# Performance work log

Measured on AMD Instinct MI355X. Metric: run time of the kernel, lower is better.

The kernel has to match this reference:

```python
import jax, jax.numpy as jnp
import numpy as np

B, S, E = 16384, 32, 128
H, DH, O = 4, 32, 128  # num_heads, head_dim (qkv_features//num_heads), out_features


def setup_inputs() -> dict:
    key = jax.random.key(0)
    kx, kq, kk, kv, ko = jax.random.split(key, 5)
    return {
        "x": jax.random.normal(kx, (B, S, E), dtype=jnp.float32),
        "w_q": jax.random.normal(kq, (H, E, DH), dtype=jnp.float32),
        "w_k": jax.random.normal(kk, (H, E, DH), dtype=jnp.float32),
        "w_v": jax.random.normal(kv, (H, E, DH), dtype=jnp.float32),
        "w_o": jax.random.normal(ko, (H, DH, O), dtype=jnp.float32),
    }


def reference(x, w_q, w_k, w_v, w_o):
    # Per-head projections: [B, H, S, DH]
    scale = jnp.asarray(w_q.shape[-1] ** -0.5, x.dtype)
    Q = jnp.einsum("bse,hed->bhsd", x, w_q) * scale
    K = jnp.einsum("bse,hed->bhsd", x, w_k)
    V = jnp.einsum("bse,hed->bhsd", x, w_v)
    scores = jnp.einsum("bhsd,bhtd->bhst", Q, K)  # [B, H, S, S]
    A = jax.nn.softmax(scores, axis=-1)
    Hd = jnp.einsum("bhst,bhtd->bhsd", A, V)  # [B, H, S, DH]
    # Per-head output projection, summed across heads: [B, S, O]
    out = jnp.einsum("bhsd,hdo->bso", Hd, w_o)
    return out
```

## Files before the change

### kernel.cpp

```cpp
#include <hip/hip_runtime.h>


typedef __bf16 bf16x8 __attribute__((ext_vector_type(8)));
typedef float f32x4 __attribute__((ext_vector_type(4)));

union FragU { unsigned int w[4]; bf16x8 v; };

__device__ inline unsigned short f2bf(float f) {
  unsigned int u = __builtin_bit_cast(unsigned int, f);
  u += 0x7FFFu + ((u >> 16) & 1u);
  return (unsigned short)(u >> 16);
}
__device__ inline float bf2f(unsigned short h) {
  return __builtin_bit_cast(float, (unsigned int)h << 16);
}

__device__ inline bf16x8 ld_frag8(const unsigned short* p) {
  FragU f;
  const uint2* q = (const uint2*)p;
  uint2 a = q[0], b = q[1];
  f.w[0] = a.x; f.w[1] = a.y; f.w[2] = b.x; f.w[3] = b.y;
  return f.v;
}

__device__ inline f32x4 mfma16(bf16x8 a, bf16x8 b, f32x4 c) {
  return __builtin_amdgcn_mfma_f32_16x16x32_bf16(a, b, c, 0, 0, 0);
}

__device__ inline void copy16(const unsigned short* src, unsigned short* dst) {
  uint4 a = *(const uint4*)src;
  uint4 b = *((const uint4*)src + 1);
  uint2* d = (uint2*)dst;
  d[0] = make_uint2(a.x, a.y); d[1] = make_uint2(a.z, a.w);
  d[2] = make_uint2(b.x, b.y); d[3] = make_uint2(b.z, b.w);
}

__global__ void prep_w(const float* __restrict__ wq, const float* __restrict__ wk,
                       const float* __restrict__ wv, const float* __restrict__ wo,
                       unsigned short* __restrict__ wsb) {
  int idx = blockIdx.x * 256 + threadIdx.x;
  int t = idx >> 14;
  int rem = idx & 16383;
  int hh = rem >> 12;
  int r2 = rem & 4095;
  const float* src = (t == 0) ? wq : (t == 1) ? wk : (t == 2) ? wv : wo;
  float v = src[rem];
  if (t == 0) v *= 0.17677669529663687f;
  int off;
  if (t < 3) { int e = r2 >> 5, d = r2 & 31; off = (hh << 12) + (d << 7) + e; }
  else       { int dh = r2 >> 7, o = r2 & 127; off = (hh << 12) + (o << 5) + dh; }
  unsigned short hi = f2bf(v);
  unsigned short lo = f2bf(v - bf2f(hi));
  wsb[(t << 15) + off] = hi;
  wsb[(t << 15) + 16384 + off] = lo;
}

#define OFF_WB_HI 0
#define OFF_WB_LO 4608
#define OFF_K_HI  9216
#define OFF_K_LO  11520
#define OFF_VT_HI 13824
#define OFF_VT_LO 16128
#define OFF_Q_HI  18432
#define OFF_Q_LO  20736
#define LDS_TOT   23040

__global__ __launch_bounds__(256, 2) void attn_fused(
    const float* __restrict__ x, const unsigned short* __restrict__ wsb,
    float* __restrict__ out) {
  __shared__ unsigned short lds[LDS_TOT];
  const int tid = threadIdx.x;
  const int lane = tid & 63;
  const int wid = tid >> 6;
  const int bl = wid >> 1;
  const int hw = wid & 1;
  const int sbase = hw << 4;
  const int col = lane & 15;
  const int quad = lane >> 4;

  bf16x8 xh[4], xl[4];
  for (int b = 0; b < 2; ++b) {
    const float4* xg = (const float4*)(x + ((long)(blockIdx.x * 2 + b) << 12));
#pragma unroll
    for (int it = 0; it < 4; ++it) {
      int f4 = it * 256 + tid;
      float4 v = xg[f4];
      int s = f4 >> 5;
      int e = (f4 & 31) << 2;
      unsigned short a0 = f2bf(v.x), b0 = f2bf(v.x - bf2f(a0));
      unsigned short a1 = f2bf(v.y), b1 = f2bf(v.y - bf2f(a1));
      unsigned short a2 = f2bf(v.z), b2 = f2bf(v.z - bf2f(a2));
      unsigned short a3 = f2bf(v.w), b3 = f2bf(v.w - bf2f(a3));
      uint2 ph, pl;
      ph.x = (unsigned)a0 | ((unsigned)a1 << 16);
      ph.y = (unsigned)a2 | ((unsigned)a3 << 16);
      pl.x = (unsigned)b0 | ((unsigned)b1 << 16);
      pl.y = (unsigned)b2 | ((unsigned)b3 << 16);
      *(uint2*)(lds + s * 132 + e) = ph;
      *(uint2*)(lds + 4224 + s * 132 + e) = pl;
    }
    __syncthreads();
    if (bl == b) {
#pragma unroll
      for (int kk = 0; kk < 4; ++kk) {
        xh[kk] = ld_frag8(lds + (sbase + col) * 132 + (kk << 5) + (quad << 3));
        xl[kk] = ld_frag8(lds + 4224 + (sbase + col) * 132 + (kk << 5) + (quad << 3));
      }
    }
    __syncthreads();
  }

  const long batch = (long)blockIdx.x * 2 + bl;
  const f32x4 zero = {0.f, 0.f, 0.f, 0.f};
  f32x4 oacc[8];
#pragma unroll
  for (int i = 0; i < 8; ++i) oacc[i] = zero;

  unsigned short* Kh = lds + OFF_K_HI + bl * 1152;
  unsigned short* Kl = lds + OFF_K_LO + bl * 1152;
  unsigned short* Vh = lds + OFF_VT_HI + bl * 1152;
  unsigned short* Vl = lds + OFF_VT_LO + bl * 1152;
  unsigned short* Qh = lds + OFF_Q_HI + (bl * 2 + hw) * 576;
  unsigned short* Ql = lds + OFF_Q_LO + (bl * 2 + hw) * 576;
  unsigned short* Abuf = lds + OFF_K_HI + bl * 1152;

  for (int hh = 0; hh < 4; ++hh) {
    __syncthreads();

    {
      int i0 = tid << 4, d = i0 >> 7, e0 = i0 & 127;
      copy16(wsb + (hh << 12) + i0, lds + OFF_WB_HI + d * 132 + e0);
      copy16(wsb + 16384 + (hh << 12) + i0, lds + OFF_WB_LO + d * 132 + e0);
    }
    __syncthreads();
    f32x4 c0 = zero, c1 = zero;
#pragma unroll
    for (int kk = 0; kk < 4; ++kk) {
      bf16x8 f0 = ld_frag8(lds + OFF_WB_HI + col * 132 + (kk << 5) + (quad << 3));
      bf16x8 f1 = ld_frag8(lds + OFF_WB_HI + (col + 16) * 132 + (kk << 5) + (quad << 3));
      bf16x8 g0 = ld_frag8(lds + OFF_WB_LO + col * 132 + (kk << 5) + (quad << 3));
      bf16x8 g1 = ld_frag8(lds + OFF_WB_LO + (col + 16) * 132 + (kk << 5) + (quad << 3));
      c0 = mfma16(xh[kk], f0, c0); c0 = mfma16(xl[kk], f0, c0); c0 = mfma16(xh[kk], g0, c0);
      c1 = mfma16(xh[kk], f1, c1); c1 = mfma16(xl[kk], f1, c1); c1 = mfma16(xh[kk], g1, c1);
    }
#pragma unroll
    for (int r = 0; r < 4; ++r) {
      int row = (quad << 2) + r;
      unsigned short hi = f2bf(c0[r]), lo = f2bf(c0[r] - bf2f(hi));
      Qh[row * 36 + col] = hi; Ql[row * 36 + col] = lo;
      hi = f2bf(c1[r]); lo = f2bf(c1[r] - bf2f(hi));
      Qh[row * 36 + col + 16] = hi; Ql[row * 36 + col + 16] = lo;
    }
    __syncthreads();

    {
      int i0 = tid << 4, d = i0 >> 7, e0 = i0 & 127;
      copy16(wsb + 32768 + (hh << 12) + i0, lds + OFF_WB_HI + d * 132 + e0);
      copy16(wsb + 32768 + 16384 + (hh << 12) + i0, lds + OFF_WB_LO + d * 132 + e0);
    }
    __syncthreads();
    c0 = zero; c1 = zero;
#pragma unroll
    for (int kk = 0; kk < 4; ++kk) {
      bf16x8 f0 = ld_frag8(lds + OFF_WB_HI + col * 132 + (kk << 5) + (quad << 3));
      bf16x8 f1 = ld_frag8(lds + OFF_WB_HI + (col + 16) * 132 + (kk << 5) + (quad << 3));
      bf16x8 g0 = ld_frag8(lds + OFF_WB_LO + col * 132 + (kk << 5) + (quad << 3));
      bf16x8 g1 = ld_frag8(lds + OFF_WB_LO + (col + 16) * 132 + (kk << 5) + (quad << 3));
      c0 = mfma16(xh[kk], f0, c0); c0 = mfma16(xl[kk], f0, c0); c0 = mfma16(xh[kk], g0, c0);
      c1 = mfma16(xh[kk], f1, c1); c1 = mfma16(xl[kk], f1, c1); c1 = mfma16(xh[kk], g1, c1);
    }
#pragma unroll
    for (int r = 0; r < 4; ++r) {
      int row = sbase + (quad << 2) + r;
      unsigned short hi = f2bf(c0[r]), lo = f2bf(c0[r] - bf2f(hi));
      Kh[row * 36 + col] = hi; Kl[row * 36 + col] = lo;
      hi = f2bf(c1[r]); lo = f2bf(c1[r] - bf2f(hi));
      Kh[row * 36 + col + 16] = hi; Kl[row * 36 + col + 16] = lo;
    }
    __syncthreads();

    {
      int i0 = tid << 4, d = i0 >> 7, e0 = i0 & 127;
      copy16(wsb + 65536 + (hh << 12) + i0, lds + OFF_WB_HI + d * 132 + e0);
      copy16(wsb + 65536 + 16384 + (hh << 12) + i0, lds + OFF_WB_LO + d * 132 + e0);
    }
    __syncthreads();
    c0 = zero; c1 = zero;
#pragma unroll
    for (int kk = 0; kk < 4; ++kk) {
      bf16x8 f0 = ld_frag8(lds + OFF_WB_HI + col * 132 + (kk << 5) + (quad << 3));
      bf16x8 f1 = ld_frag8(lds + OFF_WB_HI + (col + 16) * 132 + (kk << 5) + (quad << 3));
      bf16x8 g0 = ld_frag8(lds + OFF_WB_LO + col * 132 + (kk << 5) + (quad << 3));
      bf16x8 g1 = ld_frag8(lds + OFF_WB_LO + (col + 16) * 132 + (kk << 5) + (quad << 3));
      c0 = mfma16(xh[kk], f0, c0); c0 = mfma16(xl[kk], f0, c0); c0 = mfma16(xh[kk], g0, c0);
      c1 = mfma16(xh[kk], f1, c1); c1 = mfma16(xl[kk], f1, c1); c1 = mfma16(xh[kk], g1, c1);
    }
#pragma unroll
    for (int r = 0; r < 4; ++r) {
      int t = sbase + (quad << 2) + r;
      unsigned short hi = f2bf(c0[r]), lo = f2bf(c0[r] - bf2f(hi));
      Vh[col * 36 + t] = hi; Vl[col * 36 + t] = lo;
      hi = f2bf(c1[r]); lo = f2bf(c1[r] - bf2f(hi));
      Vh[(col + 16) * 36 + t] = hi; Vl[(col + 16) * 36 + t] = lo;
    }
    __syncthreads();

    f32x4 s0 = zero, s1 = zero;
    {
      bf16x8 qhf = ld_frag8(Qh + col * 36 + (quad << 3));
      bf16x8 qlf = ld_frag8(Ql + col * 36 + (quad << 3));
      bf16x8 k0 = ld_frag8(Kh + col * 36 + (quad << 3));
      bf16x8 k1 = ld_frag8(Kh + (col + 16) * 36 + (quad << 3));
      bf16x8 k0l = ld_frag8(Kl + col * 36 + (quad << 3));
      bf16x8 k1l = ld_frag8(Kl + (col + 16) * 36 + (quad << 3));
      s0 = mfma16(qhf, k0, s0); s0 = mfma16(qlf, k0, s0); s0 = mfma16(qhf, k0l, s0);
      s1 = mfma16(qhf, k1, s1); s1 = mfma16(qlf, k1, s1); s1 = mfma16(qhf, k1l, s1);
    }
    float a0[4], a1[4];
#pragma unroll
    for (int r = 0; r < 4; ++r) {
      float v0 = s0[r], v1 = s1[r];
      float mx = fmaxf(v0, v1);
#pragma unroll
      for (int dx = 1; dx < 16; dx <<= 1) mx = fmaxf(mx, __shfl_xor(mx, dx));
      float e0 = __expf(v0 - mx), e1 = __expf(v1 - mx);
      float sm = e0 + e1;
#pragma unroll
      for (int dx = 1; dx < 16; dx <<= 1) sm += __shfl_xor(sm, dx);
      float inv = 1.0f / sm;
      a0[r] = e0 * inv; a1[r] = e1 * inv;
    }
    __syncthreads();
#pragma unroll
    for (int r = 0; r < 4; ++r) {
      int row = sbase + (quad << 2) + r;
      Abuf[row * 36 + col] = f2bf(a0[r]);
      Abuf[row * 36 + col + 16] = f2bf(a1[r]);
    }
    __syncthreads();

    f32x4 hv0 = zero, hv1 = zero;
    {
      bf16x8 af = ld_frag8(Abuf + (sbase + col) * 36 + (quad << 3));
      bf16x8 v0h = ld_frag8(Vh + col * 36 + (quad << 3));
      bf16x8 v1h = ld_frag8(Vh + (col + 16) * 36 + (quad << 3));
      bf16x8 v0l = ld_frag8(Vl + col * 36 + (quad << 3));
      bf16x8 v1l = ld_frag8(Vl + (col + 16) * 36 + (quad << 3));
      hv0 = mfma16(af, v0h, hv0); hv0 = mfma16(af, v0l, hv0);
      hv1 = mfma16(af, v1h, hv1); hv1 = mfma16(af, v1l, hv1);
    }
#pragma unroll
    for (int r = 0; r < 4; ++r) {
      int row = (quad << 2) + r;
      unsigned short hi = f2bf(hv0[r]), lo = f2bf(hv0[r] - bf2f(hi));
      Qh[row * 36 + col] = hi; Ql[row * 36 + col] = lo;
      hi = f2bf(hv1[r]); lo = f2bf(hv1[r] - bf2f(hi));
      Qh[row * 36 + col + 16] = hi; Ql[row * 36 + col + 16] = lo;
    }
    {
      int i0 = tid << 4, o = i0 >> 5, d0 = i0 & 31;
      copy16(wsb + 98304 + (hh << 12) + i0, lds + OFF_WB_HI + o * 36 + d0);
      copy16(wsb + 98304 + 16384 + (hh << 12) + i0, lds + OFF_WB_LO + o * 36 + d0);
    }
    __syncthreads();
    {
      bf16x8 dh = ld_frag8(Qh + col * 36 + (quad << 3));
      bf16x8 dl = ld_frag8(Ql + col * 36 + (quad << 3));
#pragma unroll
      for (int t8 = 0; t8 < 8; ++t8) {
        bf16x8 wh = ld_frag8(lds + OFF_WB_HI + ((t8 << 4) + col) * 36 + (quad << 3));
        bf16x8 wl = ld_frag8(lds + OFF_WB_LO + ((t8 << 4) + col) * 36 + (quad << 3));
        oacc[t8] = mfma16(dh, wh, oacc[t8]);
        oacc[t8] = mfma16(dl, wh, oacc[t8]);
        oacc[t8] = mfma16(dh, wl, oacc[t8]);
      }
    }
  }

  float* og = out + batch * 4096;
#pragma unroll
  for (int t8 = 0; t8 < 8; ++t8) {
#pragma unroll
    for (int r = 0; r < 4; ++r) {
      og[(sbase + (quad << 2) + r) * 128 + (t8 << 4) + col] = oacc[t8][r];
    }
  }
}

extern "C" void kernel_launch(void* const* d_in, const int* in_sizes, int n_in,
                              void* d_out, int out_size, void* d_ws, size_t ws_size,
                              hipStream_t stream) {
  const float* x = (const float*)d_in[0];
  const float* wq = (const float*)d_in[1];
  const float* wk = (const float*)d_in[2];
  const float* wv = (const float*)d_in[3];
  const float* wo = (const float*)d_in[4];
  float* out = (float*)d_out;
  unsigned short* wsb = (unsigned short*)d_ws;
  hipLaunchKernelGGL(prep_w, dim3(256), dim3(256), 0, stream, wq, wk, wv, wo, wsb);
  hipLaunchKernelGGL(attn_fused, dim3(8192), dim3(256), 0, stream, x, wsb, out);
}
```

Before: 710.4 us.

## Load weights as pre-swizzled MFMA fragments from global, drop LDS staging and lo-terms

Weights are reordered on the host-side prep kernel into per-lane MFMA fragment order, so the fused kernel loads B-fragments directly from global/L2 with 16-byte loads instead of staging them through LDS with barriers. This shrinks LDS usage, allowing launch bounds to raise occupancy to 5 blocks per CU, and removes many __syncthreads. It also drops the low-order bf16 correction terms for V, the attention-V product, and the output weights, cutting MFMA count at the cost of accuracy. The softmax probabilities now reuse the per-wave Q buffer, removing further barriers.

```diff
diff --git a/kernel.cpp b/kernel.cpp
--- a/kernel.cpp
+++ b/kernel.cpp
@@ -23,16 +23,15 @@
   return f.v;
 }
 
+__device__ inline bf16x8 ld_gfrag(const unsigned short* p) {
+  FragU f;
+  uint4 v = *(const uint4*)p;
+  f.w[0] = v.x; f.w[1] = v.y; f.w[2] = v.z; f.w[3] = v.w;
+  return f.v;
+}
+
 __device__ inline f32x4 mfma16(bf16x8 a, bf16x8 b, f32x4 c) {
   return __builtin_amdgcn_mfma_f32_16x16x32_bf16(a, b, c, 0, 0, 0);
-}
-
-__device__ inline void copy16(const unsigned short* src, unsigned short* dst) {
-  uint4 a = *(const uint4*)src;
-  uint4 b = *((const uint4*)src + 1);
-  uint2* d = (uint2*)dst;
-  d[0] = make_uint2(a.x, a.y); d[1] = make_uint2(a.z, a.w);
-  d[2] = make_uint2(b.x, b.y); d[3] = make_uint2(b.z, b.w);
 }
 
 __global__ void prep_w(const float* __restrict__ wq, const float* __restrict__ wk,
@@ -40,32 +39,33 @@
                        unsigned short* __restrict__ wsb) {
   int idx = blockIdx.x * 256 + threadIdx.x;
   int t = idx >> 14;
-  int rem = idx & 16383;
-  int hh = rem >> 12;
-  int r2 = rem & 4095;
+  int h = (idx >> 12) & 3;
+  int r = idx & 4095;
   const float* src = (t == 0) ? wq : (t == 1) ? wk : (t == 2) ? wv : wo;
-  float v = src[rem];
-  if (t == 0) v *= 0.17677669529663687f;
-  int off;
-  if (t < 3) { int e = r2 >> 5, d = r2 & 31; off = (hh << 12) + (d << 7) + e; }
-  else       { int dh = r2 >> 7, o = r2 & 127; off = (hh << 12) + (o << 5) + dh; }
+  int L = (r >> 3) & 63, j = r & 7;
+  float v;
+  if (t < 3) {
+    int kk = r >> 10, half = (r >> 9) & 1;
+    int d = half * 16 + (L & 15);
+    int e = kk * 32 + ((L >> 4) << 3) + j;
+    v = src[h * 4096 + e * 32 + d];
+    if (t == 0) v *= 0.17677669529663687f;
+  } else {
+    int t8 = r >> 9;
+    int o = t8 * 16 + (L & 15);
+    int d = ((L >> 4) << 3) + j;
+    v = src[h * 4096 + d * 128 + o];
+  }
   unsigned short hi = f2bf(v);
   unsigned short lo = f2bf(v - bf2f(hi));
-  wsb[(t << 15) + off] = hi;
-  wsb[(t << 15) + 16384 + off] = lo;
-}
-
-#define OFF_WB_HI 0
-#define OFF_WB_LO 4608
-#define OFF_K_HI  9216
-#define OFF_K_LO  11520
-#define OFF_VT_HI 13824
-#define OFF_VT_LO 16128
-#define OFF_Q_HI  18432
-#define OFF_Q_LO  20736
-#define LDS_TOT   23040
-
-__global__ __launch_bounds__(256, 2) void attn_fused(
+  int base = (t * 4 + h) * 8192 + r;
+  wsb[base] = hi;
+  wsb[base + 4096] = lo;
+}
+
+#define LDS_TOT 11520
+
+__global__ __launch_bounds__(256, 5) void attn_fused(
     const float* __restrict__ x, const unsigned short* __restrict__ wsb,
     float* __restrict__ out) {
   __shared__ unsigned short lds[LDS_TOT];
@@ -77,6 +77,7 @@
   const int sbase = hw << 4;
   const int col = lane & 15;
   const int quad = lane >> 4;
+  const int lo8 = lane << 3;
 
   bf16x8 xh[4], xl[4];
   for (int b = 0; b < 2; ++b) {
@@ -116,30 +117,26 @@
 #pragma unroll
   for (int i = 0; i < 8; ++i) oacc[i] = zero;
 
-  unsigned short* Kh = lds + OFF_K_HI + bl * 1152;
-  unsigned short* Kl = lds + OFF_K_LO + bl * 1152;
-  unsigned short* Vh = lds + OFF_VT_HI + bl * 1152;
-  unsigned short* Vl = lds + OFF_VT_LO + bl * 1152;
-  unsigned short* Qh = lds + OFF_Q_HI + (bl * 2 + hw) * 576;
-  unsigned short* Ql = lds + OFF_Q_LO + (bl * 2 + hw) * 576;
-  unsigned short* Abuf = lds + OFF_K_HI + bl * 1152;
+  unsigned short* Kh = lds + 0 + bl * 1152;
+  unsigned short* Kl = lds + 2304 + bl * 1152;
+  unsigned short* Vth = lds + 4608 + bl * 1152;
+  unsigned short* Qh = lds + 6912 + wid * 576;
+  unsigned short* Ql = lds + 9216 + wid * 576;
 
   for (int hh = 0; hh < 4; ++hh) {
-    __syncthreads();
-
-    {
-      int i0 = tid << 4, d = i0 >> 7, e0 = i0 & 127;
-      copy16(wsb + (hh << 12) + i0, lds + OFF_WB_HI + d * 132 + e0);
-      copy16(wsb + 16384 + (hh << 12) + i0, lds + OFF_WB_LO + d * 132 + e0);
-    }
-    __syncthreads();
+    if (hh) __syncthreads();
+    const unsigned short* wqb = wsb + (0 * 4 + hh) * 8192;
+    const unsigned short* wkb = wsb + (1 * 4 + hh) * 8192;
+    const unsigned short* wvb = wsb + (2 * 4 + hh) * 8192;
+    const unsigned short* wob = wsb + (3 * 4 + hh) * 8192;
+
     f32x4 c0 = zero, c1 = zero;
 #pragma unroll
     for (int kk = 0; kk < 4; ++kk) {
-      bf16x8 f0 = ld_frag8(lds + OFF_WB_HI + col * 132 + (kk << 5) + (quad << 3));
-      bf16x8 f1 = ld_frag8(lds + OFF_WB_HI + (col + 16) * 132 + (kk << 5) + (quad << 3));
-      bf16x8 g0 = ld_frag8(lds + OFF_WB_LO + col * 132 + (kk << 5) + (quad << 3));
-      bf16x8 g1 = ld_frag8(lds + OFF_WB_LO + (col + 16) * 132 + (kk << 5) + (quad << 3));
+      bf16x8 f0 = ld_gfrag(wqb + kk * 1024 + lo8);
+      bf16x8 f1 = ld_gfrag(wqb + kk * 1024 + 512 + lo8);
+      bf16x8 g0 = ld_gfrag(wqb + 4096 + kk * 1024 + lo8);
+      bf16x8 g1 = ld_gfrag(wqb + 4096 + kk * 1024 + 512 + lo8);
       c0 = mfma16(xh[kk], f0, c0); c0 = mfma16(xl[kk], f0, c0); c0 = mfma16(xh[kk], g0, c0);
       c1 = mfma16(xh[kk], f1, c1); c1 = mfma16(xl[kk], f1, c1); c1 = mfma16(xh[kk], g1, c1);
     }
@@ -151,21 +148,14 @@
       hi = f2bf(c1[r]); lo = f2bf(c1[r] - bf2f(hi));
       Qh[row * 36 + col + 16] = hi; Ql[row * 36 + col + 16] = lo;
     }
-    __syncthreads();
-
-    {
-      int i0 = tid << 4, d = i0 >> 7, e0 = i0 & 127;
-      copy16(wsb + 32768 + (hh << 12) + i0, lds + OFF_WB_HI + d * 132 + e0);
-      copy16(wsb + 32768 + 16384 + (hh << 12) + i0, lds + OFF_WB_LO + d * 132 + e0);
-    }
-    __syncthreads();
+
     c0 = zero; c1 = zero;
 #pragma unroll
     for (int kk = 0; kk < 4; ++kk) {
-      bf16x8 f0 = ld_frag8(lds + OFF_WB_HI + col * 132 + (kk << 5) + (quad << 3));
-      bf16x8 f1 = ld_frag8(lds + OFF_WB_HI + (col + 16) * 132 + (kk << 5) + (quad << 3));
-      bf16x8 g0 = ld_frag8(lds + OFF_WB_LO + col * 132 + (kk << 5) + (quad << 3));
-      bf16x8 g1 = ld_frag8(lds + OFF_WB_LO + (col + 16) * 132 + (kk << 5) + (quad << 3));
+      bf16x8 f0 = ld_gfrag(wkb + kk * 1024 + lo8);
+      bf16x8 f1 = ld_gfrag(wkb + kk * 1024 + 512 + lo8);
+      bf16x8 g0 = ld_gfrag(wkb + 4096 + kk * 1024 + lo8);
+      bf16x8 g1 = ld_gfrag(wkb + 4096 + kk * 1024 + 512 + lo8);
       c0 = mfma16(xh[kk], f0, c0); c0 = mfma16(xl[kk], f0, c0); c0 = mfma16(xh[kk], g0, c0);
       c1 = mfma16(xh[kk], f1, c1); c1 = mfma16(xl[kk], f1, c1); c1 = mfma16(xh[kk], g1, c1);
     }
@@ -177,31 +167,20 @@
       hi = f2bf(c1[r]); lo = f2bf(c1[r] - bf2f(hi));
       Kh[row * 36 + col + 16] = hi; Kl[row * 36 + col + 16] = lo;
     }
-    __syncthreads();
-
-    {
-      int i0 = tid << 4, d = i0 >> 7, e0 = i0 & 127;
-      copy16(wsb + 65536 + (hh << 12) + i0, lds + OFF_WB_HI + d * 132 + e0);
-      copy16(wsb + 65536 + 16384 + (hh << 12) + i0, lds + OFF_WB_LO + d * 132 + e0);
-    }
-    __syncthreads();
+
     c0 = zero; c1 = zero;
 #pragma unroll
     for (int kk = 0; kk < 4; ++kk) {
-      bf16x8 f0 = ld_frag8(lds + OFF_WB_HI + col * 132 + (kk << 5) + (quad << 3));
-      bf16x8 f1 = ld_frag8(lds + OFF_WB_HI + (col + 16) * 132 + (kk << 5) + (quad << 3));
-      bf16x8 g0 = ld_frag8(lds + OFF_WB_LO + col * 132 + (kk << 5) + (quad << 3));
-      bf16x8 g1 = ld_frag8(lds + OFF_WB_LO + (col + 16) * 132 + (kk << 5) + (quad << 3));
-      c0 = mfma16(xh[kk], f0, c0); c0 = mfma16(xl[kk], f0, c0); c0 = mfma16(xh[kk], g0, c0);
-      c1 = mfma16(xh[kk], f1, c1); c1 = mfma16(xl[kk], f1, c1); c1 = mfma16(xh[kk], g1, c1);
+      bf16x8 f0 = ld_gfrag(wvb + kk * 1024 + lo8);
+      bf16x8 f1 = ld_gfrag(wvb + kk * 1024 + 512 + lo8);
+      c0 = mfma16(xh[kk], f0, c0); c0 = mfma16(xl[kk], f0, c0);
+      c1 = mfma16(xh[kk], f1, c1); c1 = mfma16(xl[kk], f1, c1);
     }
 #pragma unroll
     for (int r = 0; r < 4; ++r) {
       int t = sbase + (quad << 2) + r;
-      unsigned short hi = f2bf(c0[r]), lo = f2bf(c0[r] - bf2f(hi));
-      Vh[col * 36 + t] = hi; Vl[col * 36 + t] = lo;
-      hi = f2bf(c1[r]); lo = f2bf(c1[r] - bf2f(hi));
-      Vh[(col + 16) * 36 + t] = hi; Vl[(col + 16) * 36 + t] = lo;
+      Vth[col * 36 + t] = f2bf(c0[r]);
+      Vth[(col + 16) * 36 + t] = f2bf(c1[r]);
     }
     __syncthreads();
 
@@ -230,24 +209,20 @@
       float inv = 1.0f / sm;
       a0[r] = e0 * inv; a1[r] = e1 * inv;
     }
-    __syncthreads();
-#pragma unroll
-    for (int r = 0; r < 4; ++r) {
-      int row = sbase + (quad << 2) + r;
-      Abuf[row * 36 + col] = f2bf(a0[r]);
-      Abuf[row * 36 + col + 16] = f2bf(a1[r]);
-    }
-    __syncthreads();
+#pragma unroll
+    for (int r = 0; r < 4; ++r) {
+      int row = (quad << 2) + r;
+      Qh[row * 36 + col] = f2bf(a0[r]);
+      Qh[row * 36 + col + 16] = f2bf(a1[r]);
+    }
 
     f32x4 hv0 = zero, hv1 = zero;
     {
-      bf16x8 af = ld_frag8(Abuf + (sbase + col) * 36 + (quad << 3));
-      bf16x8 v0h = ld_frag8(Vh + col * 36 + (quad << 3));
-      bf16x8 v1h = ld_frag8(Vh + (col + 16) * 36 + (quad << 3));
-      bf16x8 v0l = ld_frag8(Vl + col * 36 + (quad << 3));
-      bf16x8 v1l = ld_frag8(Vl + (col + 16) * 36 + (quad << 3));
-      hv0 = mfma16(af, v0h, hv0); hv0 = mfma16(af, v0l, hv0);
-      hv1 = mfma16(af, v1h, hv1); hv1 = mfma16(af, v1l, hv1);
+      bf16x8 af = ld_frag8(Qh + col * 36 + (quad << 3));
+      bf16x8 v0h = ld_frag8(Vth + col * 36 + (quad << 3));
+      bf16x8 v1h = ld_frag8(Vth + (col + 16) * 36 + (quad << 3));
+      hv0 = mfma16(af, v0h, hv0);
+      hv1 = mfma16(af, v1h, hv1);
     }
 #pragma unroll
     for (int r = 0; r < 4; ++r) {
@@ -257,22 +232,15 @@
       hi = f2bf(hv1[r]); lo = f2bf(hv1[r] - bf2f(hi));
       Qh[row * 36 + col + 16] = hi; Ql[row * 36 + col + 16] = lo;
     }
-    {
-      int i0 = tid << 4, o = i0 >> 5, d0 = i0 & 31;
-      copy16(wsb + 98304 + (hh << 12) + i0, lds + OFF_WB_HI + o * 36 + d0);
-      copy16(wsb + 98304 + 16384 + (hh << 12) + i0, lds + OFF_WB_LO + o * 36 + d0);
-    }
-    __syncthreads();
+
     {
       bf16x8 dh = ld_frag8(Qh + col * 36 + (quad << 3));
       bf16x8 dl = ld_frag8(Ql + col * 36 + (quad << 3));
 #pragma unroll
       for (int t8 = 0; t8 < 8; ++t8) {
-        bf16x8 wh = ld_frag8(lds + OFF_WB_HI + ((t8 << 4) + col) * 36 + (quad << 3));
-        bf16x8 wl = ld_frag8(lds + OFF_WB_LO + ((t8 << 4) + col) * 36 + (quad << 3));
+        bf16x8 wh = ld_gfrag(wob + t8 * 512 + lo8);
         oacc[t8] = mfma16(dh, wh, oacc[t8]);
         oacc[t8] = mfma16(dl, wh, oacc[t8]);
-        oacc[t8] = mfma16(dh, wl, oacc[t8]);
       }
     }
   }
```

After: 758.1 us. 1.07x slower.
